# Performance work log

Measured on AMD Instinct MI355X. Metric: run time of the kernel, lower is better.

## Reference

```python
import jax, jax.numpy as jnp
import numpy as np

T, B, IN, H, L = 128, 512, 512, 512, 2


def setup_inputs() -> dict:
    key = jax.random.key(0)
    ks = jax.random.split(key, 8)
    inp = {
        "latent": jax.random.normal(ks[0], (T, B, IN), jnp.float32),
        "h0": jax.random.normal(ks[1], (L, B, H), jnp.float32),
        "c0": jax.random.normal(ks[2], (L, B, H), jnp.float32),
        "reset_mask": jax.random.randint(ks[3], (T, B), 0, 2, jnp.int32),
    }
    # LSTM params, torch layout: W_ih (4H, in), W_hh (4H, H), biases (4H,) init to 1
    for l in range(L):
        in_l = IN if l == 0 else H
        k1, k2 = jax.random.split(jax.random.fold_in(key, 100 + l))
        inp[f"W_ih{l}"] = jax.random.normal(k1, (4 * H, in_l), jnp.float32) / np.float32(np.sqrt(in_l))
        inp[f"W_hh{l}"] = jax.random.normal(k2, (4 * H, H), jnp.float32) / np.float32(np.sqrt(H))
        inp[f"b_ih{l}"] = jnp.ones((4 * H,), jnp.float32)
        inp[f"b_hh{l}"] = jnp.ones((4 * H,), jnp.float32)
    return inp


def _cell(x, h, c, W_ih, W_hh, b_ih, b_hh):
    # torch gate order: input, forget, cell(g), output
    gates = x @ W_ih.T + b_ih + h @ W_hh.T + b_hh  # (B, 4H)
    i, f, g, o = jnp.split(gates, 4, axis=-1)
    i = jax.nn.sigmoid(i)
    f = jax.nn.sigmoid(f)
    g = jnp.tanh(g)
    o = jax.nn.sigmoid(o)
    c_new = f * c + i * g
    h_new = o * jnp.tanh(c_new)
    return h_new, c_new


def reference(latent, h0, c0, reset_mask,
              W_ih0, W_hh0, b_ih0, b_hh0,
              W_ih1, W_hh1, b_ih1, b_hh1):
    def step(carry, xs):
        h, c = carry  # (L, B, H) each
        x_t, m_t = xs
        m = (m_t != 0)[None, :, None]  # (1, B, 1), broadcast over layers and H
        h = jnp.where(m, 0.0, h)
        c = jnp.where(m, 0.0, c)
        h0n, c0n = _cell(x_t, h[0], c[0], W_ih0, W_hh0, b_ih0, b_hh0)
        h1n, c1n = _cell(h0n, h[1], c[1], W_ih1, W_hh1, b_ih1, b_hh1)
        return (jnp.stack([h0n, h1n]), jnp.stack([c0n, c1n])), h1n

    (h_n, c_n), hidden = jax.lax.scan(step, (h0, c0), (latent, reset_mask))
    return hidden, h_n, c_n  # hidden: (T, B, H)
```

## Files before the change

### kernel.cpp

```cpp
#include <hip/hip_runtime.h>
#include <hip/hip_bf16.h>

typedef __hip_bfloat16 bf16;
typedef unsigned short u16;
typedef unsigned long long u64;
using frag  = __attribute__((ext_vector_type(8))) short;
using f32x4 = __attribute__((ext_vector_type(4))) float;

static constexpr int T_  = 128;
static constexpr int B_  = 512;
static constexpr int H_  = 512;
static constexpr int K_  = 512;
static constexpr int G4_ = 2048;
static constexpr int NWG = 256;

static constexpr size_t W_BYTES = 131072;
static constexpr size_t SMEM_BYTES = W_BYTES;

__device__ __forceinline__ frag ld_coh(const u16* p) {
  u64 lo = __hip_atomic_load((const u64*)p,       __ATOMIC_RELAXED, __HIP_MEMORY_SCOPE_AGENT);
  u64 hi = __hip_atomic_load((const u64*)(p + 4), __ATOMIC_RELAXED, __HIP_MEMORY_SCOPE_AGENT);
  union { u64 q[2]; frag f; } u;
  u.q[0] = lo; u.q[1] = hi;
  return u.f;
}


__global__ void k_f32_to_bf16_v4(const float4* __restrict__ src,
                                 ushort4* __restrict__ dst, int n4) {
  int i = blockIdx.x * blockDim.x + threadIdx.x;
  int stride = gridDim.x * blockDim.x;
  for (; i < n4; i += stride) {
    float4 v = src[i];
    ushort4 o;
    bf16 t0 = __float2bfloat16(v.x); o.x = *reinterpret_cast<u16*>(&t0);
    bf16 t1 = __float2bfloat16(v.y); o.y = *reinterpret_cast<u16*>(&t1);
    bf16 t2 = __float2bfloat16(v.z); o.z = *reinterpret_cast<u16*>(&t2);
    bf16 t3 = __float2bfloat16(v.w); o.w = *reinterpret_cast<u16*>(&t3);
    dst[i] = o;
  }
}

__global__ void k_bias(const float* __restrict__ bih0, const float* __restrict__ bhh0,
                       const float* __restrict__ bih1, const float* __restrict__ bhh1,
                       float* __restrict__ bsum0, float* __restrict__ bsum1) {
  int i = blockIdx.x * blockDim.x + threadIdx.x;
  if (i < G4_) {
    bsum0[i] = bih0[i] + bhh0[i];
    bsum1[i] = bih1[i] + bhh1[i];
  }
}

__global__ void k_init2(const float* __restrict__ h0,
                        u16* __restrict__ bufA0, u16* __restrict__ bufA1) {
  int i = blockIdx.x * blockDim.x + threadIdx.x;
  int n = B_ * H_;
  if (i < n) {
    bf16 a = __float2bfloat16(h0[i]);
    bf16 b = __float2bfloat16(h0[n + i]);
    bufA0[i] = *reinterpret_cast<u16*>(&a);
    bufA1[n + i] = *reinterpret_cast<u16*>(&b);
  }
}

__global__ void k_zero(int* p) {
  int i = blockIdx.x * blockDim.x + threadIdx.x;
  if (i < 256) p[i] = 0;
}

__global__ __launch_bounds__(512, 2)
void k_main(const u16* __restrict__ latb,
            const u16* __restrict__ W0i, const u16* __restrict__ W0h,
            const u16* __restrict__ W1i, const u16* __restrict__ W1h,
            const float* __restrict__ bs0, const float* __restrict__ bs1,
            const int* __restrict__ reset,
            const float* __restrict__ c0,
            u16* __restrict__ h0buf,
            u16* __restrict__ bufA0,
            u16* __restrict__ bufA1,
            float* __restrict__ hidden,
            float* __restrict__ hn,
            float* __restrict__ cn,
            int* __restrict__ arr) {
  extern __shared__ char smem_raw[];
  u16* wlds = (u16*)smem_raw;
  __shared__ float hstage[8][16][20];

  const int tid   = threadIdx.x;
  const int wg    = blockIdx.x;
  const int lb    = wg & 7;
  const int layer = lb >> 2;
  const int bg    = lb & 3;
  const int cg    = wg >> 3;
  const int hbase = cg * 16;
  const int rowbase = bg * 128;
  const int wave  = tid >> 6;
  const int lane  = tid & 63;
  const int r16   = lane & 15;
  const int kq    = lane >> 4;
  const int wrow_local = wave * 16;
  const int wrow0 = rowbase + wrow_local;

  const u16* Wih = layer ? W1i : W0i;
  const u16* Whh = layer ? W1h : W0h;
  const float* bs = layer ? bs1 : bs0;
  u16* bufA_self = layer ? bufA1 : bufA0;

  for (int it = 0; it < 16; ++it) {
    int c = it * 512 + tid;
    int fb = c >> 6, l = c & 63;
    int ni = fb >> 5, kslot = fb & 31;
    int col = hbase + (l & 15);
    int klocal = (kslot & 15) * 32 + (l >> 4) * 8;
    const u16* M = (kslot < 16) ? Wih : Whh;
    const u16* src = M + (size_t)(ni * H_ + col) * K_ + klocal;
    *(float4*)(wlds + ((size_t)c) * 8) = *(const float4*)src;
  }

  float bias[4];
  #pragma unroll
  for (int g = 0; g < 4; ++g) bias[g] = bs[g * H_ + hbase + r16];

  float creg[4];
  #pragma unroll
  for (int j = 0; j < 4; ++j)
    creg[j] = c0[((size_t)layer * B_ + (wrow0 + kq * 4 + j)) * H_ + hbase + r16];

  __syncthreads();

  for (int p = 0; p <= T_; ++p) {
    if (p) { asm volatile("buffer_inv sc0" ::: "memory"); }

    const int t = layer ? (p - 1) : p;
    const bool active = (t >= 0 && t < T_);
    float hnew_r[4], cnew_r[4];

    if (active) {
      const u16* X  = layer ? (h0buf + (size_t)(p & 1) * B_ * H_)
                            : (latb + (size_t)t * B_ * K_);
      const u16* Hp = bufA_self + (size_t)(p & 1) * B_ * H_;
      u16* HnA      = bufA_self + (size_t)((p + 1) & 1) * B_ * H_;
      u16* Hn0c     = h0buf + (size_t)((p + 1) & 1) * B_ * H_;

      const int* rst_t = reset + (size_t)t * B_;
      const int ra0 = rst_t[wrow0 + r16];
      const u16* x0  = X  + (size_t)(wrow0 + r16) * K_ + kq * 8;
      const u16* hp0 = Hp + (size_t)(wrow0 + r16) * H_ + kq * 8;

      f32x4 acc[4] = {};
      const frag zf = {};

      if (layer == 0) {
        #pragma unroll
        for (int s = 0; s < 16; ++s) {
          frag a  = *reinterpret_cast<const frag*>(x0 + s * 32);
          frag ah = ra0 ? zf : *reinterpret_cast<const frag*>(hp0 + s * 32);
          #pragma unroll
          for (int ni = 0; ni < 4; ++ni) {
            frag bx = *reinterpret_cast<const frag*>(
                wlds + ((size_t)((ni * 32 + s) * 64 + lane)) * 8);
            frag bh = *reinterpret_cast<const frag*>(
                wlds + ((size_t)((ni * 32 + 16 + s) * 64 + lane)) * 8);
            acc[ni] = __builtin_amdgcn_mfma_f32_16x16x32_bf16(a,  bx, acc[ni], 0, 0, 0);
            acc[ni] = __builtin_amdgcn_mfma_f32_16x16x32_bf16(ah, bh, acc[ni], 0, 0, 0);
          }
        }
      } else {
        #pragma unroll
        for (int s = 0; s < 16; ++s) {
          frag a  = ld_coh(x0 + s * 32);
          frag ah = ra0 ? zf : *reinterpret_cast<const frag*>(hp0 + s * 32);
          #pragma unroll
          for (int ni = 0; ni < 4; ++ni) {
            frag bx = *reinterpret_cast<const frag*>(
                wlds + ((size_t)((ni * 32 + s) * 64 + lane)) * 8);
            frag bh = *reinterpret_cast<const frag*>(
                wlds + ((size_t)((ni * 32 + 16 + s) * 64 + lane)) * 8);
            acc[ni] = __builtin_amdgcn_mfma_f32_16x16x32_bf16(a,  bx, acc[ni], 0, 0, 0);
            acc[ni] = __builtin_amdgcn_mfma_f32_16x16x32_bf16(ah, bh, acc[ni], 0, 0, 0);
          }
        }
      }

      #pragma unroll
      for (int j = 0; j < 4; ++j) {
        const int rstj = rst_t[wrow0 + kq * 4 + j];
        float gi = acc[0][j] + bias[0];
        float gf = acc[1][j] + bias[1];
        float gg = acc[2][j] + bias[2];
        float go = acc[3][j] + bias[3];
        float iv = 1.f / (1.f + __expf(-gi));
        float fv = 1.f / (1.f + __expf(-gf));
        float gv = 1.f - 2.f / (__expf(2.f * gg) + 1.f);
        float ov = 1.f / (1.f + __expf(-go));
        float ce = rstj ? 0.f : creg[j];
        float cnew = fv * ce + iv * gv;
        float hnew = ov * (1.f - 2.f / (__expf(2.f * cnew) + 1.f));
        creg[j] = cnew;
        cnew_r[j] = cnew;
        hnew_r[j] = hnew;
        hstage[wave][kq * 4 + j][r16] = hnew;
      }

      {
        const int prow = lane >> 2;
        const int pc4  = lane & 3;
        float4 v = *reinterpret_cast<const float4*>(&hstage[wave][prow][pc4 * 4]);
        bf16 b0 = __float2bfloat16(v.x), b1 = __float2bfloat16(v.y);
        bf16 b2 = __float2bfloat16(v.z), b3 = __float2bfloat16(v.w);
        u64 pk = (u64)*reinterpret_cast<u16*>(&b0)
               | ((u64)*reinterpret_cast<u16*>(&b1) << 16)
               | ((u64)*reinterpret_cast<u16*>(&b2) << 32)
               | ((u64)*reinterpret_cast<u16*>(&b3) << 48);
        const size_t hoff = (size_t)(wrow0 + prow) * H_ + hbase + pc4 * 4;
        *(u64*)(HnA + hoff) = pk;
        if (layer == 0) {
          __hip_atomic_store((u64*)(Hn0c + hoff), pk,
                             __ATOMIC_RELAXED, __HIP_MEMORY_SCOPE_AGENT);
        }
      }
    }

    if (p < T_) {
      asm volatile("s_waitcnt vmcnt(0)" ::: "memory");
      __syncthreads();
      if (tid == 0)
        __hip_atomic_store(arr + wg, p + 1, __ATOMIC_RELAXED, __HIP_MEMORY_SCOPE_AGENT);
    }

    if (active) {
      float* hidden_t = hidden + (size_t)t * B_ * H_;
      #pragma unroll
      for (int j = 0; j < 4; ++j) {
        const size_t off = (size_t)(wrow0 + kq * 4 + j) * H_ + hbase + r16;
        if (layer) hidden_t[off] = hnew_r[j];
        if (t == T_ - 1) {
          hn[(size_t)layer * B_ * H_ + off] = hnew_r[j];
          cn[(size_t)layer * B_ * H_ + off] = cnew_r[j];
        }
      }
    }

    if (p < T_) {
      if (wave == 0) {
        const int slot = (lane >> 1) * 8 + (lane & 1) * 4 + bg;
        while (__hip_atomic_load(arr + slot, __ATOMIC_RELAXED,
                                 __HIP_MEMORY_SCOPE_AGENT) < p + 1)
          __builtin_amdgcn_s_sleep(2);
      }
      __syncthreads();
    }
  }
}


extern "C" void kernel_launch(void* const* d_in, const int* in_sizes, int n_in,
                              void* d_out, int out_size, void* d_ws, size_t ws_size,
                              hipStream_t stream) {
  (void)in_sizes; (void)n_in; (void)out_size; (void)ws_size;

  const float* latent = (const float*)d_in[0];
  const float* h0in   = (const float*)d_in[1];
  const float* c0in   = (const float*)d_in[2];
  const int*   reset  = (const int*)d_in[3];
  const float* W_ih0  = (const float*)d_in[4];
  const float* W_hh0  = (const float*)d_in[5];
  const float* b_ih0  = (const float*)d_in[6];
  const float* b_hh0  = (const float*)d_in[7];
  const float* W_ih1  = (const float*)d_in[8];
  const float* W_hh1  = (const float*)d_in[9];
  const float* b_ih1  = (const float*)d_in[10];
  const float* b_hh1  = (const float*)d_in[11];

  float* out    = (float*)d_out;
  float* hidden = out;
  float* hn     = out + (size_t)T_ * B_ * H_;
  float* cn     = hn + (size_t)2 * B_ * H_;

  char* ws = (char*)d_ws;
  u16* latb  = (u16*)ws;
  u16* wih0b = latb + (size_t)T_ * B_ * K_;
  u16* whh0b = wih0b + (size_t)G4_ * K_;
  u16* wih1b = whh0b + (size_t)G4_ * K_;
  u16* whh1b = wih1b + (size_t)G4_ * K_;
  float* bsum0 = (float*)(whh1b + (size_t)G4_ * K_);
  float* bsum1 = bsum0 + G4_;
  u16* h0buf = (u16*)(bsum1 + G4_);
  u16* bufA0 = h0buf + (size_t)2 * B_ * H_;
  u16* bufA1 = bufA0 + (size_t)2 * B_ * H_;
  int* arr   = (int*)(bufA1 + (size_t)2 * B_ * H_);

  int n_lat4 = T_ * B_ * K_ / 4;
  k_f32_to_bf16_v4<<<2048, 256, 0, stream>>>((const float4*)latent, (ushort4*)latb, n_lat4);
  int n_w4 = G4_ * K_ / 4;
  k_f32_to_bf16_v4<<<256, 256, 0, stream>>>((const float4*)W_ih0, (ushort4*)wih0b, n_w4);
  k_f32_to_bf16_v4<<<256, 256, 0, stream>>>((const float4*)W_hh0, (ushort4*)whh0b, n_w4);
  k_f32_to_bf16_v4<<<256, 256, 0, stream>>>((const float4*)W_ih1, (ushort4*)wih1b, n_w4);
  k_f32_to_bf16_v4<<<256, 256, 0, stream>>>((const float4*)W_hh1, (ushort4*)whh1b, n_w4);
  k_bias<<<(G4_ + 255) / 256, 256, 0, stream>>>(b_ih0, b_hh0, b_ih1, b_hh1, bsum0, bsum1);
  k_init2<<<(B_ * H_ + 255) / 256, 256, 0, stream>>>(h0in, bufA0, bufA1);
  k_zero<<<1, 256, 0, stream>>>(arr);

  hipFuncSetAttribute((const void*)k_main, hipFuncAttributeMaxDynamicSharedMemorySize,
                      (int)SMEM_BYTES);
  void* args[] = { (void*)&latb, (void*)&wih0b, (void*)&whh0b, (void*)&wih1b, (void*)&whh1b,
                   (void*)&bsum0, (void*)&bsum1, (void*)&reset, (void*)&c0in,
                   (void*)&h0buf, (void*)&bufA0, (void*)&bufA1,
                   (void*)&hidden, (void*)&hn, (void*)&cn, (void*)&arr };
  hipLaunchCooperativeKernel((void*)k_main, dim3(NWG), dim3(512), args,
                             (unsigned int)SMEM_BYTES, stream);
}
```

Baseline: 1.563 ms.

## Switch recurrent GEMM to 32x32x16 MFMA tiles with LDS gate exchange

Replaces the per-wave 16x16x32 MFMA tiling (16 rows by four gates) with 32x32x16 MFMA tiles, where each wave pair splits a 32-row block over two gate pairs. The weight LDS layout is re-laid out to match, and accumulators go through a skewed LDS exchange buffer so each thread regains all four gates for its rows. The aim is to halve the A-operand global loads per wave and use the larger MFMA shape for throughput. In exchange it adds two extra block barriers and LDS round trips per timestep, and LDS use grows by 32KB, which may limit occupancy.

```diff
diff --git a/kernel.cpp b/kernel.cpp
--- a/kernel.cpp
+++ b/kernel.cpp
@@ -4,8 +4,8 @@
 typedef __hip_bfloat16 bf16;
 typedef unsigned short u16;
 typedef unsigned long long u64;
-using frag  = __attribute__((ext_vector_type(8))) short;
-using f32x4 = __attribute__((ext_vector_type(4))) float;
+using frag   = __attribute__((ext_vector_type(8))) short;
+using f32x16 = __attribute__((ext_vector_type(16))) float;
 
 static constexpr int T_  = 128;
 static constexpr int B_  = 512;
@@ -15,7 +15,8 @@
 static constexpr int NWG = 256;
 
 static constexpr size_t W_BYTES = 131072;
-static constexpr size_t SMEM_BYTES = W_BYTES;
+static constexpr size_t X_BYTES = 32768;
+static constexpr size_t SMEM_BYTES = W_BYTES + X_BYTES;
 
 __device__ __forceinline__ frag ld_coh(const u16* p) {
   u64 lo = __hip_atomic_load((const u64*)p,       __ATOMIC_RELAXED, __HIP_MEMORY_SCOPE_AGENT);
@@ -83,8 +84,8 @@
             float* __restrict__ cn,
             int* __restrict__ arr) {
   extern __shared__ char smem_raw[];
-  u16* wlds = (u16*)smem_raw;
-  __shared__ float hstage[8][16][20];
+  u16*   wlds = (u16*)smem_raw;
+  float* xch  = (float*)(smem_raw + W_BYTES);
 
   const int tid   = threadIdx.x;
   const int wg    = blockIdx.x;
@@ -98,8 +99,12 @@
   const int lane  = tid & 63;
   const int r16   = lane & 15;
   const int kq    = lane >> 4;
-  const int wrow_local = wave * 16;
-  const int wrow0 = rowbase + wrow_local;
+  const int c32   = lane & 31;
+  const int hi    = lane >> 5;
+  const int mi    = wave >> 1;
+  const int nj    = wave & 1;
+  const int wrow32  = rowbase + mi * 32;
+  const int wrow0_e = rowbase + mi * 32 + nj * 16;
 
   const u16* Wih = layer ? W1i : W0i;
   const u16* Whh = layer ? W1h : W0h;
@@ -109,11 +114,12 @@
   for (int it = 0; it < 16; ++it) {
     int c = it * 512 + tid;
     int fb = c >> 6, l = c & 63;
-    int ni = fb >> 5, kslot = fb & 31;
-    int col = hbase + (l & 15);
-    int klocal = (kslot & 15) * 32 + (l >> 4) * 8;
-    const u16* M = (kslot < 16) ? Wih : Whh;
-    const u16* src = M + (size_t)(ni * H_ + col) * K_ + klocal;
+    int njb = fb >> 6, s = fb & 63;
+    int gate = njb * 2 + ((l & 31) >> 4);
+    int col  = hbase + (l & 15);
+    int ksrc = (s & 31) * 16 + (l >> 5) * 8;
+    const u16* M = (s < 32) ? Wih : Whh;
+    const u16* src = M + (size_t)(gate * H_ + col) * K_ + ksrc;
     *(float4*)(wlds + ((size_t)c) * 8) = *(const float4*)src;
   }
 
@@ -124,7 +130,7 @@
   float creg[4];
   #pragma unroll
   for (int j = 0; j < 4; ++j)
-    creg[j] = c0[((size_t)layer * B_ + (wrow0 + kq * 4 + j)) * H_ + hbase + r16];
+    creg[j] = c0[((size_t)layer * B_ + (wrow0_e + kq * 4 + j)) * H_ + hbase + r16];
 
   __syncthreads();
 
@@ -143,52 +149,72 @@
       u16* Hn0c     = h0buf + (size_t)((p + 1) & 1) * B_ * H_;
 
       const int* rst_t = reset + (size_t)t * B_;
-      const int ra0 = rst_t[wrow0 + r16];
-      const u16* x0  = X  + (size_t)(wrow0 + r16) * K_ + kq * 8;
-      const u16* hp0 = Hp + (size_t)(wrow0 + r16) * H_ + kq * 8;
-
-      f32x4 acc[4] = {};
+      const int arow = wrow32 + c32;
+      const int ra = rst_t[arow];
+      const u16* xb = X  + (size_t)arow * K_ + hi * 8;
+      const u16* hb = Hp + (size_t)arow * H_ + hi * 8;
+
+      f32x16 acc = {};
       const frag zf = {};
 
       if (layer == 0) {
         #pragma unroll
-        for (int s = 0; s < 16; ++s) {
-          frag a  = *reinterpret_cast<const frag*>(x0 + s * 32);
-          frag ah = ra0 ? zf : *reinterpret_cast<const frag*>(hp0 + s * 32);
-          #pragma unroll
-          for (int ni = 0; ni < 4; ++ni) {
-            frag bx = *reinterpret_cast<const frag*>(
-                wlds + ((size_t)((ni * 32 + s) * 64 + lane)) * 8);
-            frag bh = *reinterpret_cast<const frag*>(
-                wlds + ((size_t)((ni * 32 + 16 + s) * 64 + lane)) * 8);
-            acc[ni] = __builtin_amdgcn_mfma_f32_16x16x32_bf16(a,  bx, acc[ni], 0, 0, 0);
-            acc[ni] = __builtin_amdgcn_mfma_f32_16x16x32_bf16(ah, bh, acc[ni], 0, 0, 0);
-          }
+        for (int s = 0; s < 32; ++s) {
+          frag ax = *reinterpret_cast<const frag*>(xb + s * 16);
+          frag bx = *reinterpret_cast<const frag*>(
+              wlds + ((size_t)((nj * 64 + s) * 64 + lane)) * 8);
+          acc = __builtin_amdgcn_mfma_f32_32x32x16_bf16(ax, bx, acc, 0, 0, 0);
+          frag ah = ra ? zf : *reinterpret_cast<const frag*>(hb + s * 16);
+          frag bh = *reinterpret_cast<const frag*>(
+              wlds + ((size_t)((nj * 64 + 32 + s) * 64 + lane)) * 8);
+          acc = __builtin_amdgcn_mfma_f32_32x32x16_bf16(ah, bh, acc, 0, 0, 0);
         }
       } else {
         #pragma unroll
-        for (int s = 0; s < 16; ++s) {
-          frag a  = ld_coh(x0 + s * 32);
-          frag ah = ra0 ? zf : *reinterpret_cast<const frag*>(hp0 + s * 32);
-          #pragma unroll
-          for (int ni = 0; ni < 4; ++ni) {
-            frag bx = *reinterpret_cast<const frag*>(
-                wlds + ((size_t)((ni * 32 + s) * 64 + lane)) * 8);
-            frag bh = *reinterpret_cast<const frag*>(
-                wlds + ((size_t)((ni * 32 + 16 + s) * 64 + lane)) * 8);
-            acc[ni] = __builtin_amdgcn_mfma_f32_16x16x32_bf16(a,  bx, acc[ni], 0, 0, 0);
-            acc[ni] = __builtin_amdgcn_mfma_f32_16x16x32_bf16(ah, bh, acc[ni], 0, 0, 0);
-          }
-        }
-      }
-
+        for (int s = 0; s < 32; ++s) {
+          frag ax = ld_coh(xb + s * 16);
+          frag bx = *reinterpret_cast<const frag*>(
+              wlds + ((size_t)((nj * 64 + s) * 64 + lane)) * 8);
+          acc = __builtin_amdgcn_mfma_f32_32x32x16_bf16(ax, bx, acc, 0, 0, 0);
+          frag ah = ra ? zf : *reinterpret_cast<const frag*>(hb + s * 16);
+          frag bh = *reinterpret_cast<const frag*>(
+              wlds + ((size_t)((nj * 64 + 32 + s) * 64 + lane)) * 8);
+          acc = __builtin_amdgcn_mfma_f32_32x32x16_bf16(ah, bh, acc, 0, 0, 0);
+        }
+      }
+
+      {
+        float* tb = xch + (size_t)(mi * 2 + nj) * 1024 + (size_t)c32 * 32;
+        #pragma unroll
+        for (int r = 0; r < 16; ++r) {
+          int row = (r & 3) + 8 * (r >> 2) + 4 * hi;
+          tb[(row + c32) & 31] = acc[r];
+        }
+      }
+      __syncthreads();
+
+      float gval[4][4];
+      #pragma unroll
+      for (int g = 0; g < 4; ++g) {
+        const float* tg = xch + (size_t)(mi * 2 + (g >> 1)) * 1024;
+        const int cc = (g & 1) * 16 + r16;
+        #pragma unroll
+        for (int j = 0; j < 4; ++j) {
+          int row = nj * 16 + kq * 4 + j;
+          gval[g][j] = tg[cc * 32 + ((row + cc) & 31)];
+        }
+      }
+      __syncthreads();
+
+      float* hstg = xch + (size_t)wave * 320;
       #pragma unroll
       for (int j = 0; j < 4; ++j) {
-        const int rstj = rst_t[wrow0 + kq * 4 + j];
-        float gi = acc[0][j] + bias[0];
-        float gf = acc[1][j] + bias[1];
-        float gg = acc[2][j] + bias[2];
-        float go = acc[3][j] + bias[3];
+        const int row = wrow0_e + kq * 4 + j;
+        const int rstj = rst_t[row];
+        float gi = gval[0][j] + bias[0];
+        float gf = gval[1][j] + bias[1];
+        float gg = gval[2][j] + bias[2];
+        float go = gval[3][j] + bias[3];
         float iv = 1.f / (1.f + __expf(-gi));
         float fv = 1.f / (1.f + __expf(-gf));
         float gv = 1.f - 2.f / (__expf(2.f * gg) + 1.f);
@@ -199,20 +225,20 @@
         creg[j] = cnew;
         cnew_r[j] = cnew;
         hnew_r[j] = hnew;
-        hstage[wave][kq * 4 + j][r16] = hnew;
+        hstg[(kq * 4 + j) * 20 + r16] = hnew;
       }
 
       {
         const int prow = lane >> 2;
         const int pc4  = lane & 3;
-        float4 v = *reinterpret_cast<const float4*>(&hstage[wave][prow][pc4 * 4]);
+        float4 v = *reinterpret_cast<const float4*>(hstg + prow * 20 + pc4 * 4);
         bf16 b0 = __float2bfloat16(v.x), b1 = __float2bfloat16(v.y);
         bf16 b2 = __float2bfloat16(v.z), b3 = __float2bfloat16(v.w);
         u64 pk = (u64)*reinterpret_cast<u16*>(&b0)
                | ((u64)*reinterpret_cast<u16*>(&b1) << 16)
                | ((u64)*reinterpret_cast<u16*>(&b2) << 32)
                | ((u64)*reinterpret_cast<u16*>(&b3) << 48);
-        const size_t hoff = (size_t)(wrow0 + prow) * H_ + hbase + pc4 * 4;
+        const size_t hoff = (size_t)(wrow0_e + prow) * H_ + hbase + pc4 * 4;
         *(u64*)(HnA + hoff) = pk;
         if (layer == 0) {
           __hip_atomic_store((u64*)(Hn0c + hoff), pk,
@@ -232,7 +258,7 @@
       float* hidden_t = hidden + (size_t)t * B_ * H_;
       #pragma unroll
       for (int j = 0; j < 4; ++j) {
-        const size_t off = (size_t)(wrow0 + kq * 4 + j) * H_ + hbase + r16;
+        const size_t off = (size_t)(wrow0_e + kq * 4 + j) * H_ + hbase + r16;
         if (layer) hidden_t[off] = hnew_r[j];
         if (t == T_ - 1) {
           hn[(size_t)layer * B_ * H_ + off] = hnew_r[j];
```

Measured after the change: 3.117 ms. 1.99x slower.

## Split LSTM step barrier so input GEMM overlaps wait for recurrent state

Applied to the files above, without the earlier changes.

The per-step barrier at the end of each iteration is split into finer waits. Layer 0 now computes its input projection (x·W_ih) before waiting on the recurrent h from peer workgroups, and layer 1 waits only for the layer-0 producers it needs before its input GEMM. It then waits for its own layer's recurrent producers before the h·W_hh part. This moves roughly half of the MFMA work off the critical synchronization path, at the cost of extra spin-waits and barriers per step and more delicate memory-ordering logic.

```diff
diff --git a/kernel.cpp b/kernel.cpp
--- a/kernel.cpp
+++ b/kernel.cpp
@@ -106,6 +106,10 @@
   const float* bs = layer ? bs1 : bs0;
   u16* bufA_self = layer ? bufA1 : bufA0;
 
+  const int slotPair = (lane >> 1) * 8 + (lane & 1) * 4 + bg;
+  const int slotL0   = (lane & 31) * 8 + bg;
+  const int slotL1   = (lane & 31) * 8 + 4 + bg;
+
   for (int it = 0; it < 16; ++it) {
     int c = it * 512 + tid;
     int fb = c >> 6, l = c & 63;
@@ -129,56 +133,78 @@
   __syncthreads();
 
   for (int p = 0; p <= T_; ++p) {
-    if (p) { asm volatile("buffer_inv sc0" ::: "memory"); }
-
     const int t = layer ? (p - 1) : p;
     const bool active = (t >= 0 && t < T_);
     float hnew_r[4], cnew_r[4];
+    f32x4 acc[4] = {};
+    const int* rst_t = reset + (size_t)t * B_;
+    const int ra0 = active ? rst_t[wrow0 + r16] : 0;
 
     if (active) {
-      const u16* X  = layer ? (h0buf + (size_t)(p & 1) * B_ * H_)
-                            : (latb + (size_t)t * B_ * K_);
-      const u16* Hp = bufA_self + (size_t)(p & 1) * B_ * H_;
-      u16* HnA      = bufA_self + (size_t)((p + 1) & 1) * B_ * H_;
-      u16* Hn0c     = h0buf + (size_t)((p + 1) & 1) * B_ * H_;
-
-      const int* rst_t = reset + (size_t)t * B_;
-      const int ra0 = rst_t[wrow0 + r16];
-      const u16* x0  = X  + (size_t)(wrow0 + r16) * K_ + kq * 8;
-      const u16* hp0 = Hp + (size_t)(wrow0 + r16) * H_ + kq * 8;
-
-      f32x4 acc[4] = {};
-      const frag zf = {};
-
       if (layer == 0) {
+        const u16* x0 = latb + (size_t)t * B_ * K_ + (size_t)(wrow0 + r16) * K_ + kq * 8;
         #pragma unroll
         for (int s = 0; s < 16; ++s) {
-          frag a  = *reinterpret_cast<const frag*>(x0 + s * 32);
-          frag ah = ra0 ? zf : *reinterpret_cast<const frag*>(hp0 + s * 32);
+          frag a = *reinterpret_cast<const frag*>(x0 + s * 32);
           #pragma unroll
           for (int ni = 0; ni < 4; ++ni) {
             frag bx = *reinterpret_cast<const frag*>(
                 wlds + ((size_t)((ni * 32 + s) * 64 + lane)) * 8);
-            frag bh = *reinterpret_cast<const frag*>(
-                wlds + ((size_t)((ni * 32 + 16 + s) * 64 + lane)) * 8);
-            acc[ni] = __builtin_amdgcn_mfma_f32_16x16x32_bf16(a,  bx, acc[ni], 0, 0, 0);
-            acc[ni] = __builtin_amdgcn_mfma_f32_16x16x32_bf16(ah, bh, acc[ni], 0, 0, 0);
+            acc[ni] = __builtin_amdgcn_mfma_f32_16x16x32_bf16(a, bx, acc[ni], 0, 0, 0);
           }
         }
       } else {
+        if (wave == 0) {
+          while (__hip_atomic_load(arr + slotL0, __ATOMIC_RELAXED,
+                                   __HIP_MEMORY_SCOPE_AGENT) < p)
+            __builtin_amdgcn_s_sleep(2);
+        }
+        __syncthreads();
+        const u16* x0 = h0buf + (size_t)(p & 1) * B_ * H_
+                        + (size_t)(wrow0 + r16) * H_ + kq * 8;
         #pragma unroll
         for (int s = 0; s < 16; ++s) {
-          frag a  = ld_coh(x0 + s * 32);
-          frag ah = ra0 ? zf : *reinterpret_cast<const frag*>(hp0 + s * 32);
+          frag a = ld_coh(x0 + s * 32);
           #pragma unroll
           for (int ni = 0; ni < 4; ++ni) {
             frag bx = *reinterpret_cast<const frag*>(
                 wlds + ((size_t)((ni * 32 + s) * 64 + lane)) * 8);
-            frag bh = *reinterpret_cast<const frag*>(
-                wlds + ((size_t)((ni * 32 + 16 + s) * 64 + lane)) * 8);
-            acc[ni] = __builtin_amdgcn_mfma_f32_16x16x32_bf16(a,  bx, acc[ni], 0, 0, 0);
-            acc[ni] = __builtin_amdgcn_mfma_f32_16x16x32_bf16(ah, bh, acc[ni], 0, 0, 0);
+            acc[ni] = __builtin_amdgcn_mfma_f32_16x16x32_bf16(a, bx, acc[ni], 0, 0, 0);
           }
+        }
+      }
+    }
+
+    if (wave == 0) {
+      if (layer == 0) {
+        while (__hip_atomic_load(arr + slotPair, __ATOMIC_RELAXED,
+                                 __HIP_MEMORY_SCOPE_AGENT) < p)
+          __builtin_amdgcn_s_sleep(2);
+      } else {
+        while (__hip_atomic_load(arr + slotL1, __ATOMIC_RELAXED,
+                                 __HIP_MEMORY_SCOPE_AGENT) < p)
+          __builtin_amdgcn_s_sleep(2);
+      }
+    }
+    __syncthreads();
+    asm volatile("buffer_inv sc0" ::: "memory");
+
+    if (active) {
+      const u16* Hp = bufA_self + (size_t)(p & 1) * B_ * H_;
+      u16* HnA      = bufA_self + (size_t)((p + 1) & 1) * B_ * H_;
+      u16* Hn0c     = h0buf + (size_t)((p + 1) & 1) * B_ * H_;
+
+      const u16* hp0 = Hp + (size_t)(wrow0 + r16) * H_ + kq * 8;
+      const frag zf = {};
+
+      #pragma unroll
+      for (int s = 0; s < 16; ++s) {
+        frag ah = ra0 ? zf : *reinterpret_cast<const frag*>(hp0 + s * 32);
+        #pragma unroll
+        for (int ni = 0; ni < 4; ++ni) {
+          frag bh = *reinterpret_cast<const frag*>(
+              wlds + ((size_t)((ni * 32 + 16 + s) * 64 + lane)) * 8);
+          acc[ni] = __builtin_amdgcn_mfma_f32_16x16x32_bf16(ah, bh, acc[ni], 0, 0, 0);
         }
       }
 
@@ -240,16 +266,6 @@
         }
       }
     }
-
-    if (p < T_) {
-      if (wave == 0) {
-        const int slot = (lane >> 1) * 8 + (lane & 1) * 4 + bg;
-        while (__hip_atomic_load(arr + slot, __ATOMIC_RELAXED,
-                                 __HIP_MEMORY_SCOPE_AGENT) < p + 1)
-          __builtin_amdgcn_s_sleep(2);
-      }
-      __syncthreads();
-    }
   }
 }
 
```

Measured after the change: 1.641 ms. 1.05x slower.
